# Optimization experiments

Measured on AMD Instinct MI355X. Metric: run time of the kernel, lower is better.

## Reference

```python
import jax, jax.numpy as jnp
import numpy as np

PERIODS = [4, 2, 1]   # base_periods[:n_period]
TEMPERATURE = 0.1
TOPM = 20
EPS = 1e-12


def _l2norm(v, axis):
    n = jnp.sqrt(jnp.sum(v * v, axis=axis, keepdims=True))
    return v / jnp.maximum(n, EPS)


def decompose_mg(x):
    """x: [B, L, C] -> mg: [G, B, L, C] (offset removed, as in torch code)."""
    B, L, C = x.shape
    mg = []
    for g in PERIODS:
        cur = x.reshape(B, L // g, g, C).mean(axis=2)      # unfold(size=g, step=g).mean(-1)
        cur = jnp.repeat(cur, g, axis=1)                   # repeat_interleave back to L
        mg.append(cur)
    mg = jnp.stack(mg, axis=0)                             # [G, B, L, C]
    return mg - mg[:, :, -1:, :]                           # remove per-series last-step offset


def extract_channel_state(mg):
    """mg: [G, B, L, C] -> [G, B, C, 4] (mean, std, slope, mean |diff|)."""
    L = mg.shape[2]
    mean = mg.mean(axis=2)
    std = mg.std(axis=2)                                   # unbiased=False (ddof=0)
    slope = (mg[:, :, -1, :] - mg[:, :, 0, :]) / float(L - 1)
    abs_diff = jnp.abs(mg[:, :, 1:, :] - mg[:, :, :-1, :]).mean(axis=2)
    return jnp.stack([mean, std, slope, abs_diff], axis=-1)


def setup_inputs() -> dict:
    key = jax.random.key(0)
    k1, k2, k3 = jax.random.split(key, 3)
    B, L, C, G, T, P = 32, 512, 64, 3, 10000, 96
    x = jax.random.normal(k1, (B, L, C), dtype=jnp.float32)
    pool_state = jax.random.normal(k2, (G, T, C, 4), dtype=jnp.float32)
    y_pool = jax.random.normal(k3, (T, P, C), dtype=jnp.float32)
    return {"x": x, "pool_state": pool_state, "y_pool": y_pool}


def reference(x, pool_state, y_pool):
    # Multi-scale decomposition of query batch
    q_mg = decompose_mg(x)                                  # [G, B, L, C]
    q_state = extract_channel_state(q_mg)                   # [G, B, C, 4]
    # Normalized channel-state similarity vs candidate pool
    q = _l2norm(q_state, axis=-1)
    p = _l2norm(pool_state, axis=-1)
    sim = jnp.einsum('gbcd,gtcd->gbct', q, p)               # [G, B, C, T]
    sim = sim.mean(axis=0)                                  # combine granularities -> [B, C, T]
    # Top-m retrieval per (batch, channel)
    vals, idx = jax.lax.top_k(sim, TOPM)                    # [B, C, M]
    w = jax.nn.softmax(vals / TEMPERATURE, axis=-1)         # [B, C, M]
    # Gather retrieved future windows, channelwise: y_pool [T, P, C]
    C = y_pool.shape[2]
    y_ct = jnp.transpose(y_pool, (2, 0, 1))                 # [C, T, P]
    gathered = y_ct[jnp.arange(C)[None, :, None], idx]      # [B, C, M, P]
    out = jnp.einsum('bcm,bcmp->bpc', w, gathered)          # [B, P, C]
    return out
```

## Files before the change

kernel.cpp:

```cpp
#include <hip/hip_runtime.h>
#include <math.h>

#define NB 32
#define NL 512
#define NC 64
#define NG 3
#define NT 10000
#define NP 96
#define TOPM 20
#define M1 8
#define NCH 256
#define CHUNK 40
#define QK 16
#define NCAND 64
#define GSTR ((size_t)NT * NC * 4)

__global__ __launch_bounds__(512) void pre_kernel(const float* __restrict__ x,
                                                  const float* __restrict__ ps,
                                                  double* __restrict__ q,
                                                  float* __restrict__ phat) {
  __shared__ double s_sum[8][3][64], s_sq[8][3][64], s_abs[8][3][64];
  __shared__ double s_first[3][64], s_last[3][64];
  if (blockIdx.x < NB) {
    const int b = blockIdx.x, w = threadIdx.x >> 6, c = threadIdx.x & 63;
    const float* xp = x + (size_t)b * NL * NC + c;
    const int l0 = w * 64;
    double sum[3] = {0, 0, 0}, sumsq[3] = {0, 0, 0}, sumabs[3] = {0, 0, 0};
    double prev[3] = {0, 0, 0}, first[3] = {0, 0, 0};
    if (w > 0) {
      double e0 = xp[(l0 - 4) * NC], e1 = xp[(l0 - 3) * NC];
      double e2 = xp[(l0 - 2) * NC], e3 = xp[(l0 - 1) * NC];
      prev[2] = e3; prev[1] = (e2 + e3) * 0.5; prev[0] = (e0 + e1 + e2 + e3) * 0.25;
    }
    double acc2 = 0.0, acc4 = 0.0;
    for (int i = 0; i < 64; ++i) {
      const int l = l0 + i;
      double v = (double)xp[l * NC];
      sum[2] += v; sumsq[2] += v * v;
      if (l == 0) first[2] = v; else sumabs[2] += fabs(v - prev[2]);
      prev[2] = v;
      acc2 += v;
      if (l & 1) {
        double cur = acc2 * 0.5; acc2 = 0.0;
        sum[1] += cur; sumsq[1] += cur * cur;
        if (l == 1) first[1] = cur; else sumabs[1] += fabs(cur - prev[1]);
        prev[1] = cur;
      }
      acc4 += v;
      if ((l & 3) == 3) {
        double cur = acc4 * 0.25; acc4 = 0.0;
        sum[0] += cur; sumsq[0] += cur * cur;
        if (l == 3) first[0] = cur; else sumabs[0] += fabs(cur - prev[0]);
        prev[0] = cur;
      }
    }
    for (int g = 0; g < 3; ++g) {
      s_sum[w][g][c] = sum[g]; s_sq[w][g][c] = sumsq[g]; s_abs[w][g][c] = sumabs[g];
    }
    if (w == 0) { for (int g = 0; g < 3; ++g) s_first[g][c] = first[g]; }
    if (w == 7) { for (int g = 0; g < 3; ++g) s_last[g][c] = prev[g]; }
    __syncthreads();
    if (w == 0) {
      const double J[3] = {128.0, 256.0, 512.0};
      for (int g = 0; g < 3; ++g) {
        double S = 0, Q2 = 0, A = 0;
        for (int ww = 0; ww < 8; ++ww) {
          S += s_sum[ww][g][c]; Q2 += s_sq[ww][g][c]; A += s_abs[ww][g][c];
        }
        double mean = S / J[g];
        double var = Q2 / J[g] - mean * mean; if (var < 0.0) var = 0.0;
        double last = s_last[g][c];
        double s0 = mean - last;
        double s1 = sqrt(var);
        double s2 = (last - s_first[g][c]) * (1.0 / 511.0);
        double s3 = A * (1.0 / 511.0);
        double n = sqrt(s0 * s0 + s1 * s1 + s2 * s2 + s3 * s3);
        double inv = 1.0 / fmax(n, 1e-12);
        double* qp = q + ((((size_t)g * NB) + b) * NC + c) * 4;
        qp[0] = s0 * inv; qp[1] = s1 * inv; qp[2] = s2 * inv; qp[3] = s3 * inv;
      }
    }
  } else {
    const int i = (blockIdx.x - NB) * 512 + threadIdx.x;
    if (i < NT * NC) {
      const int t = i >> 6, c = i & 63;
#pragma unroll
      for (int g = 0; g < 3; ++g) {
        const size_t off = ((((size_t)g * NT) + t) * NC + c) * 4;
        const float4 pv = *reinterpret_cast<const float4*>(ps + off);
        double p0 = pv.x, p1 = pv.y, p2 = pv.z, p3 = pv.w;
        double inv = 1.0 / fmax(sqrt(p0 * p0 + p1 * p1 + p2 * p2 + p3 * p3), 1e-12);
        float4 o;
        o.x = (float)(p0 * inv); o.y = (float)(p1 * inv);
        o.z = (float)(p2 * inv); o.w = (float)(p3 * inv);
        *reinterpret_cast<float4*>(phat + off) = o;
      }
    }
  }
}

__device__ __forceinline__ void insert8(float s, int ti, float val[M1], int idx[M1]) {
  float cv = s; int ci = ti;
#pragma unroll
  for (int m = 0; m < M1; ++m) {
    bool sw = cv > val[m];
    float tv = sw ? val[m] : cv; int tx = sw ? idx[m] : ci;
    val[m] = sw ? cv : val[m];   idx[m] = sw ? ci : idx[m];
    cv = tv; ci = tx;
  }
}

__global__ __launch_bounds__(1024, 8) void sim32_kernel(
    const float* __restrict__ phat, const double* __restrict__ q,
    float* __restrict__ cval, int* __restrict__ cidx) {
  const int wav = threadIdx.x >> 6;
  const int c = threadIdx.x & 63;
  const int b = blockIdx.x * 16 + wav;
  const int ch = blockIdx.y;
  float qv[12];
#pragma unroll
  for (int g = 0; g < 3; ++g) {
    const double* qp = q + ((((size_t)g * NB) + b) * NC + c) * 4;
#pragma unroll
    for (int j = 0; j < 4; ++j) qv[g * 4 + j] = (float)(qp[j] * (1.0 / 3.0));
  }
  float val[M1]; int idx[M1];
#pragma unroll
  for (int m = 0; m < M1; ++m) { val[m] = -1e30f; idx[m] = 0; }
  int t0 = ch * CHUNK;
  int t1 = t0 + CHUNK; if (t1 > NT) t1 = NT;
  for (int t = t0; t + 1 < t1; t += 2) {
    const size_t oA = ((size_t)t * NC + c) * 4;
    const size_t oB = ((size_t)(t + 1) * NC + c) * 4;
    const float4 a0 = *reinterpret_cast<const float4*>(phat + oA);
    const float4 a1 = *reinterpret_cast<const float4*>(phat + GSTR + oA);
    const float4 a2 = *reinterpret_cast<const float4*>(phat + 2 * GSTR + oA);
    const float4 b0 = *reinterpret_cast<const float4*>(phat + oB);
    const float4 b1 = *reinterpret_cast<const float4*>(phat + GSTR + oB);
    const float4 b2 = *reinterpret_cast<const float4*>(phat + 2 * GSTR + oB);
    float sA = qv[0] * a0.x + qv[1] * a0.y + qv[2] * a0.z + qv[3] * a0.w +
               qv[4] * a1.x + qv[5] * a1.y + qv[6] * a1.z + qv[7] * a1.w +
               qv[8] * a2.x + qv[9] * a2.y + qv[10] * a2.z + qv[11] * a2.w;
    float sB = qv[0] * b0.x + qv[1] * b0.y + qv[2] * b0.z + qv[3] * b0.w +
               qv[4] * b1.x + qv[5] * b1.y + qv[6] * b1.z + qv[7] * b1.w +
               qv[8] * b2.x + qv[9] * b2.y + qv[10] * b2.z + qv[11] * b2.w;
    if (sA > val[M1 - 1]) insert8(sA, t, val, idx);
    if (sB > val[M1 - 1]) insert8(sB, t + 1, val, idx);
  }
  float* vo = cval + ((((size_t)b * NC) + c) * NCH + ch) * M1;
  int* io = cidx + ((((size_t)b * NC) + c) * NCH + ch) * M1;
#pragma unroll
  for (int m = 0; m < M1; ++m) { vo[m] = val[m]; io[m] = idx[m]; }
}

__device__ __forceinline__ unsigned long long mk_key(float v, int t) {
  unsigned u = __float_as_uint(v);
  u = (u & 0x80000000u) ? ~u : (u | 0x80000000u);
  return ((unsigned long long)u << 32) | (unsigned long long)(0xFFFFFFFFu - (unsigned)t);
}

__global__ __launch_bounds__(128) void merge_gather_kernel(
    const float* __restrict__ cval, const int* __restrict__ cidx,
    const float* __restrict__ ps, const double* __restrict__ q,
    const float* __restrict__ y, float* __restrict__ out) {
  const int c = blockIdx.x, b = blockIdx.y;
  __shared__ float v_s[NCH * M1];
  __shared__ int i_s[NCH * M1];
  __shared__ int ct_s[NCAND];
  __shared__ double rv_s[NCAND];
  __shared__ double m0_s, inv_s;
  __shared__ double e_s[TOPM];
  __shared__ float w_s[TOPM];
  __shared__ int ts_s[TOPM];
  const int n = NCH * M1;
  const size_t row = (size_t)b * NC + c;
  const float4* vin = reinterpret_cast<const float4*>(cval + row * n);
  const int4* iin = reinterpret_cast<const int4*>(cidx + row * n);
  for (int k = threadIdx.x; k < n / 4; k += 128) {
    *reinterpret_cast<float4*>(&v_s[k * 4]) = vin[k];
    *reinterpret_cast<int4*>(&i_s[k * 4]) = iin[k];
  }
  __syncthreads();
  {
    const int w = threadIdx.x >> 6, lane = threadIdx.x & 63;
    const int lane32 = lane & 31;
    const int qtr = (w << 1) | (lane >> 5);
    const int l0 = (qtr * 64 + lane32 * 2) * M1;
    const int l1 = l0 + M1;
    int p0 = 0, p1 = 0;
    unsigned long long k0 = mk_key(v_s[l0], i_s[l0]);
    unsigned long long k1 = mk_key(v_s[l1], i_s[l1]);
    for (int r = 0; r < QK; ++r) {
      unsigned long long me = k0 > k1 ? k0 : k1;
      unsigned long long km = me;
#pragma unroll
      for (int st = 1; st < 32; st <<= 1) {
        unsigned long long k2 = __shfl_xor(km, st);
        km = k2 > km ? k2 : km;
      }
      if (lane32 == r)
        ct_s[qtr * QK + r] = (int)(0xFFFFFFFFu - (unsigned)(km & 0xFFFFFFFFull));
      if (me == km) {
        if (k0 >= k1) {
          ++p0;
          k0 = (p0 < M1) ? mk_key(v_s[l0 + p0], i_s[l0 + p0]) : 0ull;
        } else {
          ++p1;
          k1 = (p1 < M1) ? mk_key(v_s[l1 + p1], i_s[l1 + p1]) : 0ull;
        }
      }
    }
  }
  __syncthreads();
  if (threadIdx.x < NCAND) {
    const int t = ct_s[threadIdx.x];
    double s = 0.0;
#pragma unroll
    for (int g = 0; g < 3; ++g) {
      const double* qp = q + ((((size_t)g * NB) + b) * NC + c) * 4;
      const float4 pv = *reinterpret_cast<const float4*>(
          ps + ((((size_t)g * NT) + t) * NC + c) * 4);
      double pp0 = pv.x, pp1 = pv.y, pp2 = pv.z, pp3 = pv.w;
      double ss = pp0 * pp0 + pp1 * pp1 + pp2 * pp2 + pp3 * pp3;
      double dot = qp[0] * pp0 + qp[1] * pp1 + qp[2] * pp2 + qp[3] * pp3;
      s += dot / fmax(sqrt(ss), 1e-12);
    }
    rv_s[threadIdx.x] = s * (1.0 / 3.0);
  }
  __syncthreads();
  if (threadIdx.x < NCAND) {
    const double v = rv_s[threadIdx.x];
    const int t = ct_s[threadIdx.x];
    int rank = 0;
    for (int j = 0; j < NCAND; ++j) {
      double vj = rv_s[j]; int tj = ct_s[j];
      rank += (vj > v) || (vj == v && tj < t);
    }
    if (rank == 0) m0_s = v;
    __syncthreads();
    if (rank < TOPM) {
      e_s[rank] = exp((v - m0_s) * 10.0);
      ts_s[rank] = t;
    }
    __syncthreads();
    if (threadIdx.x == 0) {
      double sum = 0.0;
#pragma unroll
      for (int m = 0; m < TOPM; ++m) sum += e_s[m];
      inv_s = 1.0 / sum;
    }
    __syncthreads();
    if (threadIdx.x < TOPM) w_s[threadIdx.x] = (float)(e_s[threadIdx.x] * inv_s);
  } else {
    __syncthreads(); __syncthreads(); __syncthreads();
  }
  __syncthreads();
  const int p = threadIdx.x;
  if (p < NP) {
    float acc = 0.f;
#pragma unroll
    for (int m = 0; m < TOPM; ++m)
      acc += w_s[m] * y[(((size_t)ts_s[m]) * NP + p) * NC + c];
    out[(((size_t)b * NP) + p) * NC + c] = acc;
  }
}

__global__ __launch_bounds__(256) void sim_topk_inline_kernel(
    const float* __restrict__ ps, const double* __restrict__ q,
    double* __restrict__ cval, int* __restrict__ cidx, int nch, int chunk) {
  const int wav = threadIdx.x >> 6;
  const int c = threadIdx.x & 63;
  const int b = blockIdx.y * 4 + wav;
  const int ch = blockIdx.x;
  double qv[3][4];
#pragma unroll
  for (int g = 0; g < 3; ++g) {
    const double* qp = q + ((((size_t)g * NB) + b) * NC + c) * 4;
    qv[g][0] = qp[0]; qv[g][1] = qp[1]; qv[g][2] = qp[2]; qv[g][3] = qp[3];
  }
  double val[TOPM]; int idx[TOPM];
#pragma unroll
  for (int m = 0; m < TOPM; ++m) { val[m] = -1e300; idx[m] = 0; }
  int t0 = ch * chunk;
  int t1 = t0 + chunk; if (t1 > NT) t1 = NT;
  for (int t = t0; t < t1; ++t) {
    double s = 0.0;
#pragma unroll
    for (int g = 0; g < 3; ++g) {
      const float4 pv = *reinterpret_cast<const float4*>(
          ps + ((((size_t)g * NT) + t) * NC + c) * 4);
      double p0 = pv.x, p1 = pv.y, p2 = pv.z, p3 = pv.w;
      double ss = p0 * p0 + p1 * p1 + p2 * p2 + p3 * p3;
      double dot = qv[g][0] * p0 + qv[g][1] * p1 + qv[g][2] * p2 + qv[g][3] * p3;
      s += dot / fmax(sqrt(ss), 1e-12);
    }
    s *= (1.0 / 3.0);
    if (s > val[TOPM - 1]) {
      double cv = s; int ci = t;
#pragma unroll
      for (int m = 0; m < TOPM; ++m) {
        bool sw = cv > val[m];
        double tv = sw ? val[m] : cv; int ti = sw ? idx[m] : ci;
        val[m] = sw ? cv : val[m];    idx[m] = sw ? ci : idx[m];
        cv = tv; ci = ti;
      }
    }
  }
  double* vout = cval + ((((size_t)b * NC) + c) * nch + ch) * TOPM;
  int* iout = cidx + ((((size_t)b * NC) + c) * nch + ch) * TOPM;
#pragma unroll
  for (int m = 0; m < TOPM; ++m) { vout[m] = val[m]; iout[m] = idx[m]; }
}

__global__ __launch_bounds__(128) void merge_gather_old_kernel(
    const double* __restrict__ cval, const int* __restrict__ cidx,
    const float* __restrict__ y, float* __restrict__ out, int nch) {
  const int c = blockIdx.x;
  const int b = blockIdx.y;
  __shared__ float w_s[TOPM];
  __shared__ int i_s[TOPM];
  if (threadIdx.x == 0) {
    double val[TOPM]; int idx[TOPM];
#pragma unroll
    for (int m = 0; m < TOPM; ++m) { val[m] = -1e300; idx[m] = 0; }
    const double* vin = cval + (((size_t)b * NC) + c) * nch * TOPM;
    const int* iin = cidx + (((size_t)b * NC) + c) * nch * TOPM;
    for (int k = 0; k < nch; ++k) {
      const int base = k * TOPM;
      for (int m = 0; m < TOPM; ++m) {
        double s = vin[base + m];
        if (!(s > val[TOPM - 1])) break;
        double cv = s; int ci = iin[base + m];
#pragma unroll
        for (int mm = 0; mm < TOPM; ++mm) {
          bool sw = cv > val[mm];
          double tv = sw ? val[mm] : cv; int ti = sw ? idx[mm] : ci;
          val[mm] = sw ? cv : val[mm];   idx[mm] = sw ? ci : idx[mm];
          cv = tv; ci = ti;
        }
      }
    }
    double mx = val[0];
    double e[TOPM]; double sum = 0.0;
#pragma unroll
    for (int m = 0; m < TOPM; ++m) { e[m] = exp((val[m] - mx) * 10.0); sum += e[m]; }
    double inv = 1.0 / sum;
#pragma unroll
    for (int m = 0; m < TOPM; ++m) { w_s[m] = (float)(e[m] * inv); i_s[m] = idx[m]; }
  }
  __syncthreads();
  const int p = threadIdx.x;
  if (p < NP) {
    float acc = 0.f;
#pragma unroll
    for (int m = 0; m < TOPM; ++m)
      acc += w_s[m] * y[(((size_t)i_s[m]) * NP + p) * NC + c];
    out[(((size_t)b * NP) + p) * NC + c] = acc;
  }
}

extern "C" void kernel_launch(void* const* d_in, const int* in_sizes, int n_in,
                              void* d_out, int out_size, void* d_ws, size_t ws_size,
                              hipStream_t stream) {
  const float* x = (const float*)d_in[0];
  const float* ps = (const float*)d_in[1];
  const float* y = (const float*)d_in[2];
  float* out = (float*)d_out;
  char* ws = (char*)d_ws;

  const size_t qbytes = (size_t)NG * NB * NC * 4 * sizeof(double);
  const size_t phat32bytes = (size_t)NG * NT * NC * 4 * sizeof(float);
  const size_t cvalbytes = (size_t)NB * NC * NCH * M1 * sizeof(float);
  const size_t cidxbytes = (size_t)NB * NC * NCH * M1 * sizeof(int);

  double* qbuf = (double*)ws;

  if (ws_size >= qbytes + phat32bytes + cvalbytes + cidxbytes) {
    float* phat = (float*)(ws + qbytes);
    float* cval = (float*)(ws + qbytes + phat32bytes);
    int* cidx = (int*)((char*)cval + cvalbytes);
    const int pn_blocks = (NT * NC + 511) / 512;
    pre_kernel<<<dim3(NB + pn_blocks), dim3(512), 0, stream>>>(x, ps, qbuf, phat);
    sim32_kernel<<<dim3(NB / 16, NCH), dim3(1024), 0, stream>>>(phat, qbuf, cval, cidx);
    merge_gather_kernel<<<dim3(NC, NB), dim3(128), 0, stream>>>(cval, cidx, ps, qbuf,
                                                                y, out);
  } else {
    pre_kernel<<<dim3(NB), dim3(512), 0, stream>>>(x, ps, qbuf, (float*)nullptr);
    const size_t per_ch = (size_t)NB * NC * TOPM * (sizeof(double) + sizeof(int));
    int nch = 1;
    if (ws_size > qbytes) {
      size_t mc = (ws_size - qbytes) / per_ch;
      nch = mc < 32 ? (int)mc : 32;
      if (nch < 1) nch = 1;
    }
    const int chunk = (NT + nch - 1) / nch;
    double* cval = (double*)(ws + qbytes);
    int* cidx = (int*)((char*)cval + (size_t)NB * NC * nch * TOPM * sizeof(double));
    sim_topk_inline_kernel<<<dim3(nch, NB / 4), dim3(256), 0, stream>>>(
        ps, qbuf, cval, cidx, nch, chunk);
    merge_gather_old_kernel<<<dim3(NC, NB), dim3(128), 0, stream>>>(cval, cidx, y, out, nch);
  }
}
```

Before: 139.1 us.

## Store normalized pool state in fp16 and use packed dot2 for similarity scan

The normalized pool-state buffer is now written as fp16 (8 bytes per 4-vector instead of 16), which halves the memory read in the similarity scan. When the builtin is available, the scan computes each dot product with packed half2 fdot2 instructions that accumulate in fp32. Candidate ordering still relies on the later exact fp64 re-score of the top candidates, so the lower precision risks dropping true top-k members only near ties. The merge kernel also sorts the top-20 by pool index before gathering y, which may improve locality, and it restructures the divergent syncthreads into uniform ones.

```diff
diff --git a/kernel.cpp b/kernel.cpp
--- a/kernel.cpp
+++ b/kernel.cpp
@@ -1,4 +1,5 @@
 #include <hip/hip_runtime.h>
+#include <hip/hip_fp16.h>
 #include <math.h>
 
 #define NB 32
@@ -13,12 +14,15 @@
 #define CHUNK 40
 #define QK 16
 #define NCAND 64
-#define GSTR ((size_t)NT * NC * 4)
+#define PNBLK 1250
+#define P16STR ((size_t)NT * NC)
+
+union H2U { uint2 u; __half2 h[2]; };
 
 __global__ __launch_bounds__(512) void pre_kernel(const float* __restrict__ x,
                                                   const float* __restrict__ ps,
                                                   double* __restrict__ q,
-                                                  float* __restrict__ phat) {
+                                                  uint2* __restrict__ phat16) {
   __shared__ double s_sum[8][3][64], s_sq[8][3][64], s_abs[8][3][64];
   __shared__ double s_first[3][64], s_last[3][64];
   if (blockIdx.x < NB) {
@@ -83,17 +87,18 @@
   } else {
     const int i = (blockIdx.x - NB) * 512 + threadIdx.x;
     if (i < NT * NC) {
-      const int t = i >> 6, c = i & 63;
 #pragma unroll
       for (int g = 0; g < 3; ++g) {
-        const size_t off = ((((size_t)g * NT) + t) * NC + c) * 4;
+        const size_t off = ((size_t)g * NT * NC + i) * 4;
         const float4 pv = *reinterpret_cast<const float4*>(ps + off);
         double p0 = pv.x, p1 = pv.y, p2 = pv.z, p3 = pv.w;
         double inv = 1.0 / fmax(sqrt(p0 * p0 + p1 * p1 + p2 * p2 + p3 * p3), 1e-12);
-        float4 o;
-        o.x = (float)(p0 * inv); o.y = (float)(p1 * inv);
-        o.z = (float)(p2 * inv); o.w = (float)(p3 * inv);
-        *reinterpret_cast<float4*>(phat + off) = o;
+        H2U o;
+        o.h[0] = __halves2half2(__float2half_rn((float)(p0 * inv)),
+                                __float2half_rn((float)(p1 * inv)));
+        o.h[1] = __halves2half2(__float2half_rn((float)(p2 * inv)),
+                                __float2half_rn((float)(p3 * inv)));
+        phat16[(size_t)g * P16STR + i] = o.u;
       }
     }
   }
@@ -110,40 +115,84 @@
   }
 }
 
+#if defined(__has_builtin)
+#if __has_builtin(__builtin_amdgcn_fdot2)
+#define HAVE_FDOT2 1
+#endif
+#endif
+
+__device__ __forceinline__ float sim_dot(const uint2* __restrict__ p16,
+                                         size_t o,
+#ifdef HAVE_FDOT2
+                                         const __half2 qh[6]
+#else
+                                         const float qv[12]
+#endif
+                                         ) {
+  H2U a0, a1, a2;
+  a0.u = p16[o];
+  a1.u = p16[P16STR + o];
+  a2.u = p16[2 * P16STR + o];
+#ifdef HAVE_FDOT2
+  float s = 0.f;
+  s = __builtin_amdgcn_fdot2(qh[0], a0.h[0], s, false);
+  s = __builtin_amdgcn_fdot2(qh[1], a0.h[1], s, false);
+  s = __builtin_amdgcn_fdot2(qh[2], a1.h[0], s, false);
+  s = __builtin_amdgcn_fdot2(qh[3], a1.h[1], s, false);
+  s = __builtin_amdgcn_fdot2(qh[4], a2.h[0], s, false);
+  s = __builtin_amdgcn_fdot2(qh[5], a2.h[1], s, false);
+  return s;
+#else
+  float2 f0 = __half22float2(a0.h[0]), f1 = __half22float2(a0.h[1]);
+  float2 f2 = __half22float2(a1.h[0]), f3 = __half22float2(a1.h[1]);
+  float2 f4 = __half22float2(a2.h[0]), f5 = __half22float2(a2.h[1]);
+  return qv[0] * f0.x + qv[1] * f0.y + qv[2] * f1.x + qv[3] * f1.y +
+         qv[4] * f2.x + qv[5] * f2.y + qv[6] * f3.x + qv[7] * f3.y +
+         qv[8] * f4.x + qv[9] * f4.y + qv[10] * f5.x + qv[11] * f5.y;
+#endif
+}
+
 __global__ __launch_bounds__(1024, 8) void sim32_kernel(
-    const float* __restrict__ phat, const double* __restrict__ q,
+    const uint2* __restrict__ p16, const double* __restrict__ q,
     float* __restrict__ cval, int* __restrict__ cidx) {
   const int wav = threadIdx.x >> 6;
   const int c = threadIdx.x & 63;
   const int b = blockIdx.x * 16 + wav;
   const int ch = blockIdx.y;
-  float qv[12];
+#ifdef HAVE_FDOT2
+  __half2 qh[6];
 #pragma unroll
   for (int g = 0; g < 3; ++g) {
     const double* qp = q + ((((size_t)g * NB) + b) * NC + c) * 4;
+    qh[g * 2 + 0] = __halves2half2(__float2half_rn((float)(qp[0] * (1.0 / 3.0))),
+                                   __float2half_rn((float)(qp[1] * (1.0 / 3.0))));
+    qh[g * 2 + 1] = __halves2half2(__float2half_rn((float)(qp[2] * (1.0 / 3.0))),
+                                   __float2half_rn((float)(qp[3] * (1.0 / 3.0))));
+  }
+#else
+  float qv[12];
+#pragma unroll
+  for (int g = 0; g < 3; ++g) {
+    const double* qp = q + ((((size_t)g * NB) + b) * NC + c) * 4;
 #pragma unroll
     for (int j = 0; j < 4; ++j) qv[g * 4 + j] = (float)(qp[j] * (1.0 / 3.0));
   }
+#endif
   float val[M1]; int idx[M1];
 #pragma unroll
   for (int m = 0; m < M1; ++m) { val[m] = -1e30f; idx[m] = 0; }
   int t0 = ch * CHUNK;
   int t1 = t0 + CHUNK; if (t1 > NT) t1 = NT;
   for (int t = t0; t + 1 < t1; t += 2) {
-    const size_t oA = ((size_t)t * NC + c) * 4;
-    const size_t oB = ((size_t)(t + 1) * NC + c) * 4;
-    const float4 a0 = *reinterpret_cast<const float4*>(phat + oA);
-    const float4 a1 = *reinterpret_cast<const float4*>(phat + GSTR + oA);
-    const float4 a2 = *reinterpret_cast<const float4*>(phat + 2 * GSTR + oA);
-    const float4 b0 = *reinterpret_cast<const float4*>(phat + oB);
-    const float4 b1 = *reinterpret_cast<const float4*>(phat + GSTR + oB);
-    const float4 b2 = *reinterpret_cast<const float4*>(phat + 2 * GSTR + oB);
-    float sA = qv[0] * a0.x + qv[1] * a0.y + qv[2] * a0.z + qv[3] * a0.w +
-               qv[4] * a1.x + qv[5] * a1.y + qv[6] * a1.z + qv[7] * a1.w +
-               qv[8] * a2.x + qv[9] * a2.y + qv[10] * a2.z + qv[11] * a2.w;
-    float sB = qv[0] * b0.x + qv[1] * b0.y + qv[2] * b0.z + qv[3] * b0.w +
-               qv[4] * b1.x + qv[5] * b1.y + qv[6] * b1.z + qv[7] * b1.w +
-               qv[8] * b2.x + qv[9] * b2.y + qv[10] * b2.z + qv[11] * b2.w;
+    const size_t oA = (size_t)t * NC + c;
+    const size_t oB = oA + NC;
+#ifdef HAVE_FDOT2
+    float sA = sim_dot(p16, oA, qh);
+    float sB = sim_dot(p16, oB, qh);
+#else
+    float sA = sim_dot(p16, oA, qv);
+    float sB = sim_dot(p16, oB, qv);
+#endif
     if (sA > val[M1 - 1]) insert8(sA, t, val, idx);
     if (sB > val[M1 - 1]) insert8(sB, t + 1, val, idx);
   }
@@ -170,8 +219,9 @@
   __shared__ double rv_s[NCAND];
   __shared__ double m0_s, inv_s;
   __shared__ double e_s[TOPM];
-  __shared__ float w_s[TOPM];
   __shared__ int ts_s[TOPM];
+  __shared__ float w2_s[TOPM];
+  __shared__ int t2_s[TOPM];
   const int n = NCH * M1;
   const size_t row = (size_t)b * NC + c;
   const float4* vin = reinterpret_cast<const float4*>(cval + row * n);
@@ -202,57 +252,58 @@
         ct_s[qtr * QK + r] = (int)(0xFFFFFFFFu - (unsigned)(km & 0xFFFFFFFFull));
       if (me == km) {
         if (k0 >= k1) {
-          ++p0;
-          k0 = (p0 < M1) ? mk_key(v_s[l0 + p0], i_s[l0 + p0]) : 0ull;
+          ++p0; k0 = (p0 < M1) ? mk_key(v_s[l0 + p0], i_s[l0 + p0]) : 0ull;
         } else {
-          ++p1;
-          k1 = (p1 < M1) ? mk_key(v_s[l1 + p1], i_s[l1 + p1]) : 0ull;
+          ++p1; k1 = (p1 < M1) ? mk_key(v_s[l1 + p1], i_s[l1 + p1]) : 0ull;
         }
       }
     }
   }
   __syncthreads();
+  double myv = -1e300; int myt = 0x7fffffff;
   if (threadIdx.x < NCAND) {
-    const int t = ct_s[threadIdx.x];
+    myt = ct_s[threadIdx.x];
     double s = 0.0;
 #pragma unroll
     for (int g = 0; g < 3; ++g) {
       const double* qp = q + ((((size_t)g * NB) + b) * NC + c) * 4;
       const float4 pv = *reinterpret_cast<const float4*>(
-          ps + ((((size_t)g * NT) + t) * NC + c) * 4);
+          ps + ((((size_t)g * NT) + myt) * NC + c) * 4);
       double pp0 = pv.x, pp1 = pv.y, pp2 = pv.z, pp3 = pv.w;
       double ss = pp0 * pp0 + pp1 * pp1 + pp2 * pp2 + pp3 * pp3;
       double dot = qp[0] * pp0 + qp[1] * pp1 + qp[2] * pp2 + qp[3] * pp3;
       s += dot / fmax(sqrt(ss), 1e-12);
     }
-    rv_s[threadIdx.x] = s * (1.0 / 3.0);
-  }
-  __syncthreads();
+    myv = s * (1.0 / 3.0);
+    rv_s[threadIdx.x] = myv;
+  }
+  __syncthreads();
+  int rank = -1;
   if (threadIdx.x < NCAND) {
-    const double v = rv_s[threadIdx.x];
-    const int t = ct_s[threadIdx.x];
-    int rank = 0;
+    rank = 0;
     for (int j = 0; j < NCAND; ++j) {
       double vj = rv_s[j]; int tj = ct_s[j];
-      rank += (vj > v) || (vj == v && tj < t);
-    }
-    if (rank == 0) m0_s = v;
-    __syncthreads();
-    if (rank < TOPM) {
-      e_s[rank] = exp((v - m0_s) * 10.0);
-      ts_s[rank] = t;
-    }
-    __syncthreads();
-    if (threadIdx.x == 0) {
-      double sum = 0.0;
-#pragma unroll
-      for (int m = 0; m < TOPM; ++m) sum += e_s[m];
-      inv_s = 1.0 / sum;
-    }
-    __syncthreads();
-    if (threadIdx.x < TOPM) w_s[threadIdx.x] = (float)(e_s[threadIdx.x] * inv_s);
-  } else {
-    __syncthreads(); __syncthreads(); __syncthreads();
+      rank += (vj > myv) || (vj == myv && tj < myt);
+    }
+    if (rank == 0) m0_s = myv;
+  }
+  __syncthreads();
+  if (rank >= 0 && rank < TOPM) { e_s[rank] = exp((myv - m0_s) * 10.0); ts_s[rank] = myt; }
+  __syncthreads();
+  if (threadIdx.x == 0) {
+    double sum = 0.0;
+#pragma unroll
+    for (int m = 0; m < TOPM; ++m) sum += e_s[m];
+    inv_s = 1.0 / sum;
+  }
+  __syncthreads();
+  if (threadIdx.x < TOPM) {
+    const int t = ts_s[threadIdx.x];
+    int pos = 0;
+#pragma unroll
+    for (int j = 0; j < TOPM; ++j) pos += (ts_s[j] < t);
+    w2_s[pos] = (float)(e_s[threadIdx.x] * inv_s);
+    t2_s[pos] = t;
   }
   __syncthreads();
   const int p = threadIdx.x;
@@ -260,7 +311,7 @@
     float acc = 0.f;
 #pragma unroll
     for (int m = 0; m < TOPM; ++m)
-      acc += w_s[m] * y[(((size_t)ts_s[m]) * NP + p) * NC + c];
+      acc += w2_s[m] * y[(((size_t)t2_s[m]) * NP + p) * NC + c];
     out[(((size_t)b * NP) + p) * NC + c] = acc;
   }
 }
@@ -369,23 +420,23 @@
   char* ws = (char*)d_ws;
 
   const size_t qbytes = (size_t)NG * NB * NC * 4 * sizeof(double);
-  const size_t phat32bytes = (size_t)NG * NT * NC * 4 * sizeof(float);
+  const size_t phat16bytes = (size_t)NG * NT * NC * 8;
   const size_t cvalbytes = (size_t)NB * NC * NCH * M1 * sizeof(float);
-  const size_t cidxbytes = (size_t)NB * NC * NCH * M1 * sizeof(int);
+  const size_t cidxbytes = cvalbytes;
 
   double* qbuf = (double*)ws;
 
-  if (ws_size >= qbytes + phat32bytes + cvalbytes + cidxbytes) {
-    float* phat = (float*)(ws + qbytes);
-    float* cval = (float*)(ws + qbytes + phat32bytes);
+  if (ws_size >= qbytes + phat16bytes + cvalbytes + cidxbytes) {
+    uint2* phat16 = (uint2*)(ws + qbytes);
+    float* cval = (float*)(ws + qbytes + phat16bytes);
     int* cidx = (int*)((char*)cval + cvalbytes);
-    const int pn_blocks = (NT * NC + 511) / 512;
-    pre_kernel<<<dim3(NB + pn_blocks), dim3(512), 0, stream>>>(x, ps, qbuf, phat);
-    sim32_kernel<<<dim3(NB / 16, NCH), dim3(1024), 0, stream>>>(phat, qbuf, cval, cidx);
-    merge_gather_kernel<<<dim3(NC, NB), dim3(128), 0, stream>>>(cval, cidx, ps, qbuf,
-                                                                y, out);
+    pre_kernel<<<dim3(NB + PNBLK), dim3(512), 0, stream>>>(x, ps, qbuf, phat16);
+    sim32_kernel<<<dim3(NB / 16, NCH), dim3(1024), 0, stream>>>(phat16, qbuf,
+                                                                cval, cidx);
+    merge_gather_kernel<<<dim3(NC, NB), dim3(128), 0, stream>>>(cval, cidx, ps,
+                                                                qbuf, y, out);
   } else {
-    pre_kernel<<<dim3(NB), dim3(512), 0, stream>>>(x, ps, qbuf, (float*)nullptr);
+    pre_kernel<<<dim3(NB), dim3(512), 0, stream>>>(x, ps, qbuf, (uint2*)nullptr);
     const size_t per_ch = (size_t)NB * NC * TOPM * (sizeof(double) + sizeof(int));
     int nch = 1;
     if (ws_size > qbytes) {
@@ -394,10 +445,11 @@
       if (nch < 1) nch = 1;
     }
     const int chunk = (NT + nch - 1) / nch;
-    double* cval = (double*)(ws + qbytes);
-    int* cidx = (int*)((char*)cval + (size_t)NB * NC * nch * TOPM * sizeof(double));
+    double* fcval = (double*)(ws + qbytes);
+    int* fcidx = (int*)((char*)fcval + (size_t)NB * NC * nch * TOPM * sizeof(double));
     sim_topk_inline_kernel<<<dim3(nch, NB / 4), dim3(256), 0, stream>>>(
-        ps, qbuf, cval, cidx, nch, chunk);
-    merge_gather_old_kernel<<<dim3(NC, NB), dim3(128), 0, stream>>>(cval, cidx, y, out, nch);
-  }
-}
+        ps, qbuf, fcval, fcidx, nch, chunk);
+    merge_gather_old_kernel<<<dim3(NC, NB), dim3(128), 0, stream>>>(fcval, fcidx, y,
+                                                                    out, nch);
+  }
+}
```

Result: slower. 144.2 us (+3.6%).
